# Performance work log

Hardware: AMD Instinct MI355X
Metric: run time of the kernel (lower is better)

## Reference

```python
import jax, jax.numpy as jnp
import numpy as np

B, T, N, H, F, E = 8, 64, 2048, 64, 64, 32768
G = 3 * H  # GRU gate dim


def setup_inputs() -> dict:
    key = jax.random.key(0)
    ks = jax.random.split(key, 12)
    s = 0.05
    return {
        "x": jax.random.normal(ks[0], (B, T, N, F), jnp.float32),
        "targets": jax.random.normal(ks[1], (B, T, N, 1), jnp.float32),
        "targets_mask": jax.random.uniform(ks[2], (B, T, N, 1)) > 0.2,
        "edge_index": jax.random.randint(ks[3], (2, E), 0, N),
        "W_msg": jax.random.normal(ks[4], (H, H), jnp.float32) * s,
        "b_msg": jnp.zeros((H,), jnp.float32),
        "W_mix": jax.random.normal(ks[5], (H, H + F), jnp.float32) * s,
        "b_mix": jnp.zeros((H,), jnp.float32),
        "W_ih": jax.random.normal(ks[6], (N, G, H), jnp.float32) * s,
        "W_hh": jax.random.normal(ks[7], (N, G, H), jnp.float32) * s,
        "b_ih": jnp.zeros((N, G), jnp.float32),
        "b_hh": jnp.zeros((N, G), jnp.float32),
        "W_read": jax.random.normal(ks[8], (1, H), jnp.float32) * s,
        "b_read": jnp.zeros((1,), jnp.float32),
    }


def reference(x, targets, targets_mask, edge_index,
              W_msg, b_msg, W_mix, b_mix,
              W_ih, W_hh, b_ih, b_hh, W_read, b_read):
    src, dst = edge_index[0], edge_index[1]

    def step(state, x_t):
        # state: [B,N,H], x_t: [B,N,F]
        m = jnp.einsum('bnh,gh->bng', state, W_msg) + b_msg           # state_to_message
        agg = jnp.zeros_like(m).at[:, dst, :].add(m[:, src, :])       # add-aggregate over directed edges
        mi = jnp.concatenate([agg, x_t], axis=-1)                     # [B,N,H+F]
        m2 = jnp.einsum('bnf,hf->bnh', mi, W_mix) + b_mix             # mix_input
        # per-node independent GRU cells (batched weights [N,3H,*])
        gi = jnp.einsum('bnh,ngh->bng', m2, W_ih) + b_ih
        gh = jnp.einsum('bnh,ngh->bng', state, W_hh) + b_hh
        i_r, i_z, i_n = jnp.split(gi, 3, axis=-1)
        h_r, h_z, h_n = jnp.split(gh, 3, axis=-1)
        r = jax.nn.sigmoid(i_r + h_r)
        z = jax.nn.sigmoid(i_z + h_z)
        n_cand = jnp.tanh(i_n + r * h_n)
        new_state = (1.0 - z) * n_cand + z * state
        out = jnp.einsum('bnh,oh->bno', new_state, W_read) + b_read   # readout -> [B,N,1]
        return new_state, out

    state0 = jnp.zeros((B, N, H), x.dtype)
    _, outs = jax.lax.scan(step, state0, jnp.swapaxes(x, 0, 1))       # outs: [T,B,N,1]
    outputs = jnp.swapaxes(outs, 0, 1)                                # [B,T,N,1]
    loss = 0.5 * (outputs - targets) ** 2
    mask = targets_mask.astype(loss.dtype)
    return jnp.sum(loss * mask) / jnp.sum(mask)                       # masked mean
```

## Files before the change

kernel.cpp:

```cpp
#include <hip/hip_runtime.h>
#include <math.h>

namespace {
constexpr int B = 8, T = 64, N = 2048, H = 64, F = 64, E = 32768, G = 192;
constexpr int BNH = B * N * H;
constexpr int NWELEM = N * G * H;
constexpr int NBLK = 1024;
}

typedef __attribute__((ext_vector_type(8))) short bfrag;
typedef __attribute__((ext_vector_type(4))) float ffrag;
typedef long f8frag;

#define MFMA(a, b, c)  __builtin_amdgcn_mfma_f32_16x16x32_bf16(a, b, c, 0, 0, 0)
#define MFMA8(a, b, c) __builtin_amdgcn_mfma_f32_16x16x32_fp8_fp8(a, b, c, 0, 0, 0)

#define DS (1.f / 512.f)

__device__ __forceinline__ unsigned short f2bf(float f) {
  unsigned u = __float_as_uint(f);
  u += 0x7fffu + ((u >> 16) & 1u);
  return (unsigned short)(u >> 16);
}
__device__ __forceinline__ float bf2f(unsigned short u) {
  return __uint_as_float(((unsigned)u) << 16);
}
template<bool HI>
__device__ __forceinline__ unsigned cvtpk8(float a, float b, unsigned old) {
  return __builtin_amdgcn_cvt_pk_fp8_f32(a, b, old, HI);
}

__device__ __forceinline__ void grid_bar(int* bar, int t) {
  __syncthreads();
  if (threadIdx.x == 0) {
    __hip_atomic_fetch_add(&bar[(blockIdx.x & 63) * 16], 1,
                           __ATOMIC_RELAXED, __HIP_MEMORY_SCOPE_AGENT);
  }
  if (blockIdx.x == 0) {
    if (threadIdx.x < 64) {
      while (__hip_atomic_load(&bar[threadIdx.x * 16],
                               __ATOMIC_RELAXED, __HIP_MEMORY_SCOPE_AGENT) < 16 * (t + 1))
        __builtin_amdgcn_s_sleep(1);
      if (threadIdx.x == 0)
        __hip_atomic_store(&bar[4096], t + 1, __ATOMIC_RELAXED, __HIP_MEMORY_SCOPE_AGENT);
    }
  } else if (threadIdx.x == 0) {
    while (__hip_atomic_load(&bar[4096], __ATOMIC_RELAXED, __HIP_MEMORY_SCOPE_AGENT) < t + 1)
      __builtin_amdgcn_s_sleep(2);
  }
  asm volatile("" ::: "memory");
  __syncthreads();
}


__global__ __launch_bounds__(256) void init_kernel(
    unsigned short* __restrict__ buf0, const float* __restrict__ b_msg,
    float* __restrict__ loss_acc, float* __restrict__ scal,
    int* __restrict__ deg, int* __restrict__ bar)
{
  int stride = gridDim.x * blockDim.x;
  for (int i = blockIdx.x * blockDim.x + threadIdx.x; i < BNH; i += stride) {
    buf0[i] = f2bf(b_msg[i & (H - 1)]);
    if (i < 8192) bar[i] = 0;
    if (i < N) { loss_acc[i] = 0.f; deg[i] = 0; }
    if (i < 16) scal[i] = 0.f;
  }
}

__global__ __launch_bounds__(256) void conv_kernel(
    const float* __restrict__ Wi, const float* __restrict__ Wh,
    const float* __restrict__ Wm, const float* __restrict__ Wg,
    unsigned char* __restrict__ Wib, unsigned char* __restrict__ Whb,
    unsigned short* __restrict__ Wmb, unsigned short* __restrict__ Wgb)
{
  int stride = gridDim.x * blockDim.x * 2;
  for (int i = (blockIdx.x * blockDim.x + threadIdx.x) * 2; i < NWELEM; i += stride) {
    unsigned p = cvtpk8<false>(Wi[i] * 32.f, Wi[i + 1] * 32.f, 0u);
    *(unsigned short*)(Wib + i) = (unsigned short)p;
    p = cvtpk8<false>(Wh[i] * 32.f, Wh[i + 1] * 32.f, 0u);
    *(unsigned short*)(Whb + i) = (unsigned short)p;
    if (i < 64 * 128) { Wmb[i] = f2bf(Wm[i]); Wmb[i + 1] = f2bf(Wm[i + 1]); }
    if (i < 64 * 64)  { Wgb[i] = f2bf(Wg[i]); Wgb[i + 1] = f2bf(Wg[i + 1]); }
  }
}

__global__ __launch_bounds__(256) void hist_kernel(const int* __restrict__ ei, int* __restrict__ deg) {
  int e = blockIdx.x * 256 + threadIdx.x;
  if (e < E) atomicAdd(&deg[ei[E + e]], 1);
}

__global__ __launch_bounds__(1024) void scan_kernel(const int* __restrict__ deg,
    int* __restrict__ row_ptr, int* __restrict__ cursor)
{
  __shared__ int s[N];
  int tid = threadIdx.x;
  s[tid] = deg[tid];
  s[tid + 1024] = deg[tid + 1024];
  __syncthreads();
  for (int off = 1; off < N; off <<= 1) {
    int v0 = (tid >= off) ? s[tid - off] : 0;
    int v1 = s[tid + 1024 - off];
    __syncthreads();
    s[tid] += v0;
    s[tid + 1024] += v1;
    __syncthreads();
  }
  row_ptr[tid + 1] = s[tid];
  row_ptr[tid + 1025] = s[tid + 1024];
  cursor[tid] = (tid == 0) ? 0 : s[tid - 1];
  cursor[tid + 1024] = s[tid + 1023];
  if (tid == 0) row_ptr[0] = 0;
}

__global__ __launch_bounds__(256) void fill_kernel(const int* __restrict__ ei,
    int* __restrict__ cursor, int* __restrict__ col_src)
{
  int e = blockIdx.x * 256 + threadIdx.x;
  if (e < E) {
    int d = ei[E + e];
    int slot = atomicAdd(&cursor[d], 1);
    col_src[slot] = ei[e];
  }
}

__global__ __launch_bounds__(256) void mask_kernel(const int* __restrict__ mask, float* __restrict__ scal) {
  int stride = gridDim.x * blockDim.x;
  int v = 0;
  for (int i = blockIdx.x * blockDim.x + threadIdx.x; i < B * T * N; i += stride)
    v += (mask[i] != 0);
  for (int o = 1; o < 64; o <<= 1) v += __shfl_xor(v, o, 64);
  if ((threadIdx.x & 63) == 0) atomicAdd(&scal[0], (float)v);
}


__global__ __attribute__((amdgpu_flat_work_group_size(256, 256), amdgpu_waves_per_eu(4, 4)))
void persist_kernel(
    const float* __restrict__ x, const float* __restrict__ targets,
    const int* __restrict__ mask,
    const unsigned char* __restrict__ W_ihb, const unsigned char* __restrict__ W_hhb,
    const unsigned short* __restrict__ W_mixb, const unsigned short* __restrict__ W_msgb,
    const float* __restrict__ b_ih, const float* __restrict__ b_hh,
    const float* __restrict__ b_mix, const float* __restrict__ b_msg,
    const float* __restrict__ W_read, const float* __restrict__ b_read,
    const int* __restrict__ row_ptr, const int* __restrict__ col_src,
    unsigned short* bufs,
    float* __restrict__ loss_acc, int* __restrict__ bar)
{
  __shared__ float sts[2][8][64];
  __shared__ float partial[4][8][72];
  __shared__ unsigned char m2F8[8 * 80];
  __shared__ unsigned short nsA[8 * 72];
  __shared__ float redS[4][8];

  const int tid = threadIdx.x;
  const int w = tid >> 6, lane = tid & 63;
  const int mrow = lane & 15, quad = lane >> 4;
  const int n0 = blockIdx.x * 2;
  const bfrag za = (bfrag)0;
  const int hcol = w * 16 + mrow;

  f8frag whf[2][6], wif[2][6];
#pragma unroll
  for (int k = 0; k < 2; ++k) {
    const unsigned char* Wh = W_hhb + (size_t)(n0 + k) * (G * H);
    const unsigned char* Wi = W_ihb + (size_t)(n0 + k) * (G * H);
#pragma unroll
    for (int tt = 0; tt < 3; ++tt) {
      const int off = ((w + tt * 4) * 16 + mrow) * H + quad * 8;
      whf[k][2 * tt]     = *(const f8frag*)(Wh + off);
      whf[k][2 * tt + 1] = *(const f8frag*)(Wh + off + 32);
      wif[k][2 * tt]     = *(const f8frag*)(Wi + off);
      wif[k][2 * tt + 1] = *(const f8frag*)(Wi + off + 32);
    }
  }
  const unsigned short* wmp = W_mixb + hcol * 128 + quad * 8;
  const unsigned short* wgp = W_msgb + hcol * H + quad * 8;

  float bir[2], biz[2], bin_[2], bhr[2], bhz[2], bhn[2];
#pragma unroll
  for (int k = 0; k < 2; ++k) {
    const int bg = (n0 + k) * G + hcol;
    bir[k] = b_ih[bg]; biz[k] = b_ih[bg + 64]; bin_[k] = b_ih[bg + 128];
    bhr[k] = b_hh[bg]; bhz[k] = b_hh[bg + 64]; bhn[k] = b_hh[bg + 128];
  }
  float wrd = W_read[hcol];
  float bmix = b_mix[hcol];
  float bmsg = b_msg[hcol];
  const float brd = b_read[0];
  const int e0a = row_ptr[n0], e0b = row_ptr[n0 + 1], e0c = row_ptr[n0 + 2];

#pragma unroll
  for (int k = 0; k < 2; ++k) {
#pragma unroll
    for (int j = 0; j < 6; ++j) {
      asm volatile("" : "+v"(whf[k][j]));
      asm volatile("" : "+v"(wif[k][j]));
    }
    asm volatile("" : "+v"(bir[k]), "+v"(biz[k]), "+v"(bin_[k]),
                      "+v"(bhr[k]), "+v"(bhz[k]), "+v"(bhn[k]));
  }
  asm volatile("" : "+v"(wrd), "+v"(bmix), "+v"(bmsg));

  for (int i = tid; i < 2 * 8 * 64; i += 256) ((float*)sts)[i] = 0.f;
  __syncthreads();

  float lsum[2] = {0.f, 0.f};
  const unsigned short* mcur = bufs;
  unsigned short* mnxt = bufs + BNH;

#pragma unroll 1
  for (int t = 0; t < T; ++t) {
#pragma unroll
    for (int k = 0; k < 2; ++k) {
      const int nn = n0 + k;
      const int ee0 = k ? e0b : e0a;
      const int ee1 = k ? e0c : e0b;

      bfrag wm0 = *(const bfrag*)(wmp);
      bfrag wm1 = *(const bfrag*)(wmp + 32);
      bfrag wm2 = *(const bfrag*)(wmp + 64);
      bfrag wm3 = *(const bfrag*)(wmp + 96);
      f8frag asF0 = 0, asF1 = 0;
      bfrag a2 = za, a3 = za;
      if (mrow < 8) {
        const float* sp = &sts[k][mrow][0];
        {
          float4 s0 = *(const float4*)(sp + quad * 8);
          float4 s1 = *(const float4*)(sp + quad * 8 + 4);
          unsigned u0 = 0, u1 = 0;
          u0 = cvtpk8<false>(s0.x * 16.f, s0.y * 16.f, u0);
          u0 = cvtpk8<true >(s0.z * 16.f, s0.w * 16.f, u0);
          u1 = cvtpk8<false>(s1.x * 16.f, s1.y * 16.f, u1);
          u1 = cvtpk8<true >(s1.z * 16.f, s1.w * 16.f, u1);
          asF0 = (f8frag)(((unsigned long long)u1 << 32) | u0);
          s0 = *(const float4*)(sp + 32 + quad * 8);
          s1 = *(const float4*)(sp + 32 + quad * 8 + 4);
          u0 = 0; u1 = 0;
          u0 = cvtpk8<false>(s0.x * 16.f, s0.y * 16.f, u0);
          u0 = cvtpk8<true >(s0.z * 16.f, s0.w * 16.f, u0);
          u1 = cvtpk8<false>(s1.x * 16.f, s1.y * 16.f, u1);
          u1 = cvtpk8<true >(s1.z * 16.f, s1.w * 16.f, u1);
          asF1 = (f8frag)(((unsigned long long)u1 << 32) | u0);
        }
        const float* xp = x + (((size_t)mrow * T + t) * N + nn) * F;
        {
          float4 t0 = *(const float4*)(xp + quad * 8);
          float4 t1 = *(const float4*)(xp + quad * 8 + 4);
          a2[0]=(short)f2bf(t0.x); a2[1]=(short)f2bf(t0.y); a2[2]=(short)f2bf(t0.z); a2[3]=(short)f2bf(t0.w);
          a2[4]=(short)f2bf(t1.x); a2[5]=(short)f2bf(t1.y); a2[6]=(short)f2bf(t1.z); a2[7]=(short)f2bf(t1.w);
          t0 = *(const float4*)(xp + 32 + quad * 8);
          t1 = *(const float4*)(xp + 32 + quad * 8 + 4);
          a3[0]=(short)f2bf(t0.x); a3[1]=(short)f2bf(t0.y); a3[2]=(short)f2bf(t0.z); a3[3]=(short)f2bf(t0.w);
          a3[4]=(short)f2bf(t1.x); a3[5]=(short)f2bf(t1.y); a3[6]=(short)f2bf(t1.z); a3[7]=(short)f2bf(t1.w);
        }
      }
      {
        float accL[4] = {0.f,0.f,0.f,0.f}, accH[4] = {0.f,0.f,0.f,0.f};
        const int j = lane & 31, bh = lane >> 5;
        const unsigned* mcU = (const unsigned*)mcur;
        for (int e = ee0 + w; e < ee1; e += 4) {
          const unsigned* mp = mcU + (size_t)col_src[e] * 256 + bh * 32 + j;
#pragma unroll
          for (int bb = 0; bb < 4; ++bb) {
            unsigned v = mp[bb * 64];
            accL[bb] += bf2f((unsigned short)(v & 0xffffu));
            accH[bb] += bf2f((unsigned short)(v >> 16));
          }
        }
#pragma unroll
        for (int bb = 0; bb < 4; ++bb) {
          partial[w][bb * 2 + bh][2 * j]     = accL[bb];
          partial[w][bb * 2 + bh][2 * j + 1] = accH[bb];
        }
      }
      ffrag ah0 = {0.f,0.f,0.f,0.f}, ah1 = {0.f,0.f,0.f,0.f}, ah2 = {0.f,0.f,0.f,0.f};
      ah0 = MFMA8(asF0, whf[k][0], ah0); ah0 = MFMA8(asF1, whf[k][1], ah0);
      ah1 = MFMA8(asF0, whf[k][2], ah1); ah1 = MFMA8(asF1, whf[k][3], ah1);
      ah2 = MFMA8(asF0, whf[k][4], ah2); ah2 = MFMA8(asF1, whf[k][5], ah2);
      __syncthreads();

      {
        bfrag a0 = za, a1 = za;
        if (mrow < 8) {
          const float* p = &partial[0][mrow][quad * 8];
#pragma unroll
          for (int j = 0; j < 8; ++j) {
            float s = p[j] + p[j + 576] + p[j + 1152] + p[j + 1728];
            a0[j] = (short)f2bf(s);
          }
          const float* p2 = &partial[0][mrow][32 + quad * 8];
#pragma unroll
          for (int j = 0; j < 8; ++j) {
            float s = p2[j] + p2[j + 576] + p2[j + 1152] + p2[j + 1728];
            a1[j] = (short)f2bf(s);
          }
        }
        ffrag accm = {0.f, 0.f, 0.f, 0.f};
        accm = MFMA(a0, wm0, accm);
        accm = MFMA(a1, wm1, accm);
        accm = MFMA(a2, wm2, accm);
        accm = MFMA(a3, wm3, accm);
        if (quad < 2) {
#pragma unroll
          for (int r = 0; r < 4; ++r) {
            unsigned p = cvtpk8<false>((accm[r] + bmix) * 16.f, 0.f, 0u);
            m2F8[(quad * 4 + r) * 80 + hcol] = (unsigned char)(p & 0xffu);
          }
        }
      }
      __syncthreads();

      bfrag wg0 = *(const bfrag*)(wgp);
      bfrag wg1 = *(const bfrag*)(wgp + 32);
      {
        f8frag amF0 = 0, amF1 = 0;
        if (mrow < 8) {
          amF0 = *(const f8frag*)&m2F8[mrow * 80 + quad * 8];
          amF1 = *(const f8frag*)&m2F8[mrow * 80 + 32 + quad * 8];
        }
        ffrag ai0 = {0.f,0.f,0.f,0.f}, ai1 = {0.f,0.f,0.f,0.f}, ai2 = {0.f,0.f,0.f,0.f};
        ai0 = MFMA8(amF0, wif[k][0], ai0); ai0 = MFMA8(amF1, wif[k][1], ai0);
        ai1 = MFMA8(amF0, wif[k][2], ai1); ai1 = MFMA8(amF1, wif[k][3], ai1);
        ai2 = MFMA8(amF0, wif[k][4], ai2); ai2 = MFMA8(amF1, wif[k][5], ai2);
        if (quad < 2) {
          float v[4];
#pragma unroll
          for (int r = 0; r < 4; ++r) {
            const int b = quad * 4 + r;
            float rs  = (ai0[r] + ah0[r]) * DS + bir[k] + bhr[k];
            float zs  = (ai1[r] + ah1[r]) * DS + biz[k] + bhz[k];
            float in_ = ai2[r] * DS + bin_[k];
            float hn  = ah2[r] * DS + bhn[k];
            float rg = 1.f / (1.f + __expf(-rs));
            float z  = 1.f / (1.f + __expf(-zs));
            float pre = in_ + rg * hn;
            float a = __expf(-2.f * fabsf(pre));
            float nc = copysignf((1.f - a) / (1.f + a), pre);
            float sold = sts[k][b][hcol];
            float ns = (1.f - z) * nc + z * sold;
            sts[k][b][hcol] = ns;
            nsA[b * 72 + hcol] = f2bf(ns);
            v[r] = ns * wrd;
          }
#pragma unroll
          for (int o = 1; o < 16; o <<= 1) {
#pragma unroll
            for (int r = 0; r < 4; ++r) v[r] += __shfl_xor(v[r], o, 64);
          }
          if (mrow == 0) {
#pragma unroll
            for (int r = 0; r < 4; ++r) redS[w][quad * 4 + r] = v[r];
          }
        }
      }
      __syncthreads();

      {
        bfrag an0 = za, an1 = za;
        if (mrow < 8) {
          an0 = *(const bfrag*)&nsA[mrow * 72 + quad * 8];
          an1 = *(const bfrag*)&nsA[mrow * 72 + 32 + quad * 8];
        }
        ffrag accg = {0.f, 0.f, 0.f, 0.f};
        accg = MFMA(an0, wg0, accg);
        accg = MFMA(an1, wg1, accg);
        if (quad < 2) {
          unsigned* mnU = (unsigned*)mnxt;
          const int jcol = hcol >> 1;
#pragma unroll
          for (int r = 0; r < 4; ++r) {
            float v0 = accg[r] + bmsg;
            float v1 = __shfl_xor(v0, 1, 64);
            if (!(mrow & 1)) {
              unsigned pk = (unsigned)f2bf(v0) | ((unsigned)f2bf(v1) << 16);
              __hip_atomic_store(&mnU[(size_t)nn * 256 + (quad * 4 + r) * 32 + jcol],
                                 pk, __ATOMIC_RELAXED, __HIP_MEMORY_SCOPE_AGENT);
            }
          }
        }
      }
      if (tid < 8) {
        float vv = redS[0][tid] + redS[1][tid] + redS[2][tid] + redS[3][tid] + brd;
        size_t idx = ((size_t)tid * T + t) * N + nn;
        float d = vv - targets[idx];
        float l = (mask[idx] != 0) ? 0.5f * d * d : 0.f;
        l += __shfl_xor(l, 1, 64);
        l += __shfl_xor(l, 2, 64);
        l += __shfl_xor(l, 4, 64);
        if (tid == 0) lsum[k] += l;
      }
    }
    grid_bar(bar, t);
    mcur = mnxt;
    mnxt += BNH;
  }
  if (tid == 0) { loss_acc[n0] = lsum[0]; loss_acc[n0 + 1] = lsum[1]; }
}

__global__ __launch_bounds__(256) void final_kernel(const float* __restrict__ loss_acc,
    const float* __restrict__ scal, float* __restrict__ out)
{
  __shared__ float sred[4];
  float v = 0.f;
  for (int i = threadIdx.x; i < N; i += 256) v += loss_acc[i];
  for (int o = 1; o < 64; o <<= 1) v += __shfl_xor(v, o, 64);
  if ((threadIdx.x & 63) == 0) sred[threadIdx.x >> 6] = v;
  __syncthreads();
  if (threadIdx.x == 0) out[0] = (sred[0] + sred[1] + sred[2] + sred[3]) / scal[0];
}

extern "C" void kernel_launch(void* const* d_in, const int* in_sizes, int n_in,
                              void* d_out, int out_size, void* d_ws, size_t ws_size,
                              hipStream_t stream)
{
  const float* x       = (const float*)d_in[0];
  const float* targets = (const float*)d_in[1];
  const int*   mask    = (const int*)d_in[2];
  const int*   ei      = (const int*)d_in[3];
  const float* W_msg   = (const float*)d_in[4];
  const float* b_msg   = (const float*)d_in[5];
  const float* W_mix   = (const float*)d_in[6];
  const float* b_mix   = (const float*)d_in[7];
  const float* W_ih    = (const float*)d_in[8];
  const float* W_hh    = (const float*)d_in[9];
  const float* b_ih    = (const float*)d_in[10];
  const float* b_hh    = (const float*)d_in[11];
  const float* W_read  = (const float*)d_in[12];
  const float* b_read  = (const float*)d_in[13];
  float* out = (float*)d_out;

  unsigned short* bufs  = (unsigned short*)d_ws;
  float* loss_acc       = (float*)(bufs + (size_t)(T + 1) * BNH);
  float* scal           = loss_acc + N;
  int* deg              = (int*)(scal + 16);
  int* row_ptr          = deg + N;
  int* cursor           = row_ptr + (N + 16);
  int* col_src          = cursor + N;
  int* bar              = col_src + E;
  unsigned char* W_ihb  = (unsigned char*)(bar + 8192);
  unsigned char* W_hhb  = W_ihb + NWELEM;
  unsigned short* W_mixb = (unsigned short*)(W_hhb + NWELEM);
  unsigned short* W_msgb = W_mixb + 64 * 128;

  init_kernel<<<1024, 256, 0, stream>>>(bufs, b_msg, loss_acc, scal, deg, bar);
  conv_kernel<<<8192, 256, 0, stream>>>(W_ih, W_hh, W_mix, W_msg, W_ihb, W_hhb, W_mixb, W_msgb);
  hist_kernel<<<E / 256, 256, 0, stream>>>(ei, deg);
  scan_kernel<<<1, 1024, 0, stream>>>(deg, row_ptr, cursor);
  fill_kernel<<<E / 256, 256, 0, stream>>>(ei, cursor, col_src);
  mask_kernel<<<512, 256, 0, stream>>>(mask, scal);

  persist_kernel<<<NBLK, 256, 0, stream>>>(x, targets, mask,
                                           W_ihb, W_hhb, W_mixb, W_msgb,
                                           b_ih, b_hh, b_mix, b_msg, W_read, b_read,
                                           row_ptr, col_src, bufs, loss_acc, bar);

  final_kernel<<<1, 256, 0, stream>>>(loss_acc, scal, out);
}
```

Before: 2.180 ms.

## Process both nodes per block together to halve block barriers per step

Restructures each time step so the two nodes a block owns are processed in lockstep, with double-buffered shared staging (m2F8, nsA, redS). Each phase now covers both nodes, cutting the __syncthreads count per step from six to three. Edge gathering is split so two waves serve each node, and the x loads for both nodes are issued at the start of the step. The cost is higher register pressure from holding both nodes' fragments and accumulators, at a fixed 4-waves-per-EU occupancy.

```diff
diff --git a/kernel.cpp b/kernel.cpp
--- a/kernel.cpp
+++ b/kernel.cpp
@@ -148,9 +148,9 @@
 {
   __shared__ float sts[2][8][64];
   __shared__ float partial[4][8][72];
-  __shared__ unsigned char m2F8[8 * 80];
-  __shared__ unsigned short nsA[8 * 72];
-  __shared__ float redS[4][8];
+  __shared__ unsigned char m2F8[2][8 * 80];
+  __shared__ unsigned short nsA[2][8 * 72];
+  __shared__ float redS[2][4][8];
 
   const int tid = threadIdx.x;
   const int w = tid >> 6, lane = tid & 63;
@@ -204,162 +204,179 @@
   for (int i = tid; i < 2 * 8 * 64; i += 256) ((float*)sts)[i] = 0.f;
   __syncthreads();
 
-  float lsum[2] = {0.f, 0.f};
+  float lsum0 = 0.f, lsum1 = 0.f;
   const unsigned short* mcur = bufs;
   unsigned short* mnxt = bufs + BNH;
 
 #pragma unroll 1
   for (int t = 0; t < T; ++t) {
+    float4 xt[2][4];
+    if (mrow < 8) {
+#pragma unroll
+      for (int k = 0; k < 2; ++k) {
+        const float* xp = x + (((size_t)mrow * T + t) * N + (n0 + k)) * F;
+        xt[k][0] = *(const float4*)(xp + quad * 8);
+        xt[k][1] = *(const float4*)(xp + quad * 8 + 4);
+        xt[k][2] = *(const float4*)(xp + 32 + quad * 8);
+        xt[k][3] = *(const float4*)(xp + 32 + quad * 8 + 4);
+      }
+    }
+    {
+      const int kk = w >> 1, ws = w & 1;
+      const int ge0 = (kk ? e0b : e0a) + ws;
+      const int ge1 = kk ? e0c : e0b;
+      float accL[4] = {0.f,0.f,0.f,0.f}, accH[4] = {0.f,0.f,0.f,0.f};
+      const int j = lane & 31, bh = lane >> 5;
+      const unsigned* mcU = (const unsigned*)mcur;
+      for (int e = ge0; e < ge1; e += 2) {
+        const unsigned* mp = mcU + (size_t)col_src[e] * 256 + bh * 32 + j;
+#pragma unroll
+        for (int bb = 0; bb < 4; ++bb) {
+          unsigned v = mp[bb * 64];
+          accL[bb] += bf2f((unsigned short)(v & 0xffffu));
+          accH[bb] += bf2f((unsigned short)(v >> 16));
+        }
+      }
+#pragma unroll
+      for (int bb = 0; bb < 4; ++bb) {
+        partial[w][bb * 2 + bh][2 * j]     = accL[bb];
+        partial[w][bb * 2 + bh][2 * j + 1] = accH[bb];
+      }
+    }
+    f8frag asF[2][2];
+    bfrag a2[2], a3[2];
+#pragma unroll
+    for (int k = 0; k < 2; ++k) { asF[k][0] = 0; asF[k][1] = 0; a2[k] = za; a3[k] = za; }
+    if (mrow < 8) {
+#pragma unroll
+      for (int k = 0; k < 2; ++k) {
+        const float* sp = &sts[k][mrow][0];
+        float4 s0 = *(const float4*)(sp + quad * 8);
+        float4 s1 = *(const float4*)(sp + quad * 8 + 4);
+        unsigned u0 = 0, u1 = 0;
+        u0 = cvtpk8<false>(s0.x * 16.f, s0.y * 16.f, u0);
+        u0 = cvtpk8<true >(s0.z * 16.f, s0.w * 16.f, u0);
+        u1 = cvtpk8<false>(s1.x * 16.f, s1.y * 16.f, u1);
+        u1 = cvtpk8<true >(s1.z * 16.f, s1.w * 16.f, u1);
+        asF[k][0] = (f8frag)(((unsigned long long)u1 << 32) | u0);
+        s0 = *(const float4*)(sp + 32 + quad * 8);
+        s1 = *(const float4*)(sp + 32 + quad * 8 + 4);
+        u0 = 0; u1 = 0;
+        u0 = cvtpk8<false>(s0.x * 16.f, s0.y * 16.f, u0);
+        u0 = cvtpk8<true >(s0.z * 16.f, s0.w * 16.f, u0);
+        u1 = cvtpk8<false>(s1.x * 16.f, s1.y * 16.f, u1);
+        u1 = cvtpk8<true >(s1.z * 16.f, s1.w * 16.f, u1);
+        asF[k][1] = (f8frag)(((unsigned long long)u1 << 32) | u0);
+        a2[k][0]=(short)f2bf(xt[k][0].x); a2[k][1]=(short)f2bf(xt[k][0].y);
+        a2[k][2]=(short)f2bf(xt[k][0].z); a2[k][3]=(short)f2bf(xt[k][0].w);
+        a2[k][4]=(short)f2bf(xt[k][1].x); a2[k][5]=(short)f2bf(xt[k][1].y);
+        a2[k][6]=(short)f2bf(xt[k][1].z); a2[k][7]=(short)f2bf(xt[k][1].w);
+        a3[k][0]=(short)f2bf(xt[k][2].x); a3[k][1]=(short)f2bf(xt[k][2].y);
+        a3[k][2]=(short)f2bf(xt[k][2].z); a3[k][3]=(short)f2bf(xt[k][2].w);
+        a3[k][4]=(short)f2bf(xt[k][3].x); a3[k][5]=(short)f2bf(xt[k][3].y);
+        a3[k][6]=(short)f2bf(xt[k][3].z); a3[k][7]=(short)f2bf(xt[k][3].w);
+      }
+    }
+    ffrag ah[2][3];
 #pragma unroll
     for (int k = 0; k < 2; ++k) {
-      const int nn = n0 + k;
-      const int ee0 = k ? e0b : e0a;
-      const int ee1 = k ? e0c : e0b;
-
+      ah[k][0] = (ffrag){0.f,0.f,0.f,0.f};
+      ah[k][1] = (ffrag){0.f,0.f,0.f,0.f};
+      ah[k][2] = (ffrag){0.f,0.f,0.f,0.f};
+      ah[k][0] = MFMA8(asF[k][0], whf[k][0], ah[k][0]);
+      ah[k][0] = MFMA8(asF[k][1], whf[k][1], ah[k][0]);
+      ah[k][1] = MFMA8(asF[k][0], whf[k][2], ah[k][1]);
+      ah[k][1] = MFMA8(asF[k][1], whf[k][3], ah[k][1]);
+      ah[k][2] = MFMA8(asF[k][0], whf[k][4], ah[k][2]);
+      ah[k][2] = MFMA8(asF[k][1], whf[k][5], ah[k][2]);
+    }
+    __syncthreads();
+
+    {
       bfrag wm0 = *(const bfrag*)(wmp);
       bfrag wm1 = *(const bfrag*)(wmp + 32);
       bfrag wm2 = *(const bfrag*)(wmp + 64);
       bfrag wm3 = *(const bfrag*)(wmp + 96);
-      f8frag asF0 = 0, asF1 = 0;
-      bfrag a2 = za, a3 = za;
-      if (mrow < 8) {
-        const float* sp = &sts[k][mrow][0];
-        {
-          float4 s0 = *(const float4*)(sp + quad * 8);
-          float4 s1 = *(const float4*)(sp + quad * 8 + 4);
-          unsigned u0 = 0, u1 = 0;
-          u0 = cvtpk8<false>(s0.x * 16.f, s0.y * 16.f, u0);
-          u0 = cvtpk8<true >(s0.z * 16.f, s0.w * 16.f, u0);
-          u1 = cvtpk8<false>(s1.x * 16.f, s1.y * 16.f, u1);
-          u1 = cvtpk8<true >(s1.z * 16.f, s1.w * 16.f, u1);
-          asF0 = (f8frag)(((unsigned long long)u1 << 32) | u0);
-          s0 = *(const float4*)(sp + 32 + quad * 8);
-          s1 = *(const float4*)(sp + 32 + quad * 8 + 4);
-          u0 = 0; u1 = 0;
-          u0 = cvtpk8<false>(s0.x * 16.f, s0.y * 16.f, u0);
-          u0 = cvtpk8<true >(s0.z * 16.f, s0.w * 16.f, u0);
-          u1 = cvtpk8<false>(s1.x * 16.f, s1.y * 16.f, u1);
-          u1 = cvtpk8<true >(s1.z * 16.f, s1.w * 16.f, u1);
-          asF1 = (f8frag)(((unsigned long long)u1 << 32) | u0);
-        }
-        const float* xp = x + (((size_t)mrow * T + t) * N + nn) * F;
-        {
-          float4 t0 = *(const float4*)(xp + quad * 8);
-          float4 t1 = *(const float4*)(xp + quad * 8 + 4);
-          a2[0]=(short)f2bf(t0.x); a2[1]=(short)f2bf(t0.y); a2[2]=(short)f2bf(t0.z); a2[3]=(short)f2bf(t0.w);
-          a2[4]=(short)f2bf(t1.x); a2[5]=(short)f2bf(t1.y); a2[6]=(short)f2bf(t1.z); a2[7]=(short)f2bf(t1.w);
-          t0 = *(const float4*)(xp + 32 + quad * 8);
-          t1 = *(const float4*)(xp + 32 + quad * 8 + 4);
-          a3[0]=(short)f2bf(t0.x); a3[1]=(short)f2bf(t0.y); a3[2]=(short)f2bf(t0.z); a3[3]=(short)f2bf(t0.w);
-          a3[4]=(short)f2bf(t1.x); a3[5]=(short)f2bf(t1.y); a3[6]=(short)f2bf(t1.z); a3[7]=(short)f2bf(t1.w);
-        }
-      }
-      {
-        float accL[4] = {0.f,0.f,0.f,0.f}, accH[4] = {0.f,0.f,0.f,0.f};
-        const int j = lane & 31, bh = lane >> 5;
-        const unsigned* mcU = (const unsigned*)mcur;
-        for (int e = ee0 + w; e < ee1; e += 4) {
-          const unsigned* mp = mcU + (size_t)col_src[e] * 256 + bh * 32 + j;
-#pragma unroll
-          for (int bb = 0; bb < 4; ++bb) {
-            unsigned v = mp[bb * 64];
-            accL[bb] += bf2f((unsigned short)(v & 0xffffu));
-            accH[bb] += bf2f((unsigned short)(v >> 16));
-          }
-        }
-#pragma unroll
-        for (int bb = 0; bb < 4; ++bb) {
-          partial[w][bb * 2 + bh][2 * j]     = accL[bb];
-          partial[w][bb * 2 + bh][2 * j + 1] = accH[bb];
-        }
-      }
-      ffrag ah0 = {0.f,0.f,0.f,0.f}, ah1 = {0.f,0.f,0.f,0.f}, ah2 = {0.f,0.f,0.f,0.f};
-      ah0 = MFMA8(asF0, whf[k][0], ah0); ah0 = MFMA8(asF1, whf[k][1], ah0);
-      ah1 = MFMA8(asF0, whf[k][2], ah1); ah1 = MFMA8(asF1, whf[k][3], ah1);
-      ah2 = MFMA8(asF0, whf[k][4], ah2); ah2 = MFMA8(asF1, whf[k][5], ah2);
-      __syncthreads();
-
-      {
+#pragma unroll
+      for (int k = 0; k < 2; ++k) {
         bfrag a0 = za, a1 = za;
         if (mrow < 8) {
-          const float* p = &partial[0][mrow][quad * 8];
-#pragma unroll
-          for (int j = 0; j < 8; ++j) {
-            float s = p[j] + p[j + 576] + p[j + 1152] + p[j + 1728];
-            a0[j] = (short)f2bf(s);
-          }
-          const float* p2 = &partial[0][mrow][32 + quad * 8];
-#pragma unroll
-          for (int j = 0; j < 8; ++j) {
-            float s = p2[j] + p2[j + 576] + p2[j + 1152] + p2[j + 1728];
-            a1[j] = (short)f2bf(s);
-          }
+          const float* p = &partial[2 * k][mrow][quad * 8];
+#pragma unroll
+          for (int j = 0; j < 8; ++j) a0[j] = (short)f2bf(p[j] + p[j + 576]);
+          const float* p2 = &partial[2 * k][mrow][32 + quad * 8];
+#pragma unroll
+          for (int j = 0; j < 8; ++j) a1[j] = (short)f2bf(p2[j] + p2[j + 576]);
         }
         ffrag accm = {0.f, 0.f, 0.f, 0.f};
         accm = MFMA(a0, wm0, accm);
         accm = MFMA(a1, wm1, accm);
-        accm = MFMA(a2, wm2, accm);
-        accm = MFMA(a3, wm3, accm);
+        accm = MFMA(a2[k], wm2, accm);
+        accm = MFMA(a3[k], wm3, accm);
         if (quad < 2) {
 #pragma unroll
           for (int r = 0; r < 4; ++r) {
             unsigned p = cvtpk8<false>((accm[r] + bmix) * 16.f, 0.f, 0u);
-            m2F8[(quad * 4 + r) * 80 + hcol] = (unsigned char)(p & 0xffu);
+            m2F8[k][(quad * 4 + r) * 80 + hcol] = (unsigned char)(p & 0xffu);
           }
         }
       }
-      __syncthreads();
-
+    }
+    __syncthreads();
+
+#pragma unroll
+    for (int k = 0; k < 2; ++k) {
+      f8frag amF0 = 0, amF1 = 0;
+      if (mrow < 8) {
+        amF0 = *(const f8frag*)&m2F8[k][mrow * 80 + quad * 8];
+        amF1 = *(const f8frag*)&m2F8[k][mrow * 80 + 32 + quad * 8];
+      }
+      ffrag ai0 = {0.f,0.f,0.f,0.f}, ai1 = {0.f,0.f,0.f,0.f}, ai2 = {0.f,0.f,0.f,0.f};
+      ai0 = MFMA8(amF0, wif[k][0], ai0); ai0 = MFMA8(amF1, wif[k][1], ai0);
+      ai1 = MFMA8(amF0, wif[k][2], ai1); ai1 = MFMA8(amF1, wif[k][3], ai1);
+      ai2 = MFMA8(amF0, wif[k][4], ai2); ai2 = MFMA8(amF1, wif[k][5], ai2);
+      if (quad < 2) {
+        float v[4];
+#pragma unroll
+        for (int r = 0; r < 4; ++r) {
+          const int b = quad * 4 + r;
+          float rs  = (ai0[r] + ah[k][0][r]) * DS + bir[k] + bhr[k];
+          float zs  = (ai1[r] + ah[k][1][r]) * DS + biz[k] + bhz[k];
+          float in_ = ai2[r] * DS + bin_[k];
+          float hn  = ah[k][2][r] * DS + bhn[k];
+          float rg = 1.f / (1.f + __expf(-rs));
+          float z  = 1.f / (1.f + __expf(-zs));
+          float pre = in_ + rg * hn;
+          float a = __expf(-2.f * fabsf(pre));
+          float nc = copysignf((1.f - a) / (1.f + a), pre);
+          float sold = sts[k][b][hcol];
+          float ns = (1.f - z) * nc + z * sold;
+          sts[k][b][hcol] = ns;
+          nsA[k][b * 72 + hcol] = f2bf(ns);
+          v[r] = ns * wrd;
+        }
+#pragma unroll
+        for (int o = 1; o < 16; o <<= 1) {
+#pragma unroll
+          for (int r = 0; r < 4; ++r) v[r] += __shfl_xor(v[r], o, 64);
+        }
+        if (mrow == 0) {
+#pragma unroll
+          for (int r = 0; r < 4; ++r) redS[k][w][quad * 4 + r] = v[r];
+        }
+      }
+    }
+    __syncthreads();
+
+    {
       bfrag wg0 = *(const bfrag*)(wgp);
       bfrag wg1 = *(const bfrag*)(wgp + 32);
-      {
-        f8frag amF0 = 0, amF1 = 0;
-        if (mrow < 8) {
-          amF0 = *(const f8frag*)&m2F8[mrow * 80 + quad * 8];
-          amF1 = *(const f8frag*)&m2F8[mrow * 80 + 32 + quad * 8];
-        }
-        ffrag ai0 = {0.f,0.f,0.f,0.f}, ai1 = {0.f,0.f,0.f,0.f}, ai2 = {0.f,0.f,0.f,0.f};
-        ai0 = MFMA8(amF0, wif[k][0], ai0); ai0 = MFMA8(amF1, wif[k][1], ai0);
-        ai1 = MFMA8(amF0, wif[k][2], ai1); ai1 = MFMA8(amF1, wif[k][3], ai1);
-        ai2 = MFMA8(amF0, wif[k][4], ai2); ai2 = MFMA8(amF1, wif[k][5], ai2);
-        if (quad < 2) {
-          float v[4];
-#pragma unroll
-          for (int r = 0; r < 4; ++r) {
-            const int b = quad * 4 + r;
-            float rs  = (ai0[r] + ah0[r]) * DS + bir[k] + bhr[k];
-            float zs  = (ai1[r] + ah1[r]) * DS + biz[k] + bhz[k];
-            float in_ = ai2[r] * DS + bin_[k];
-            float hn  = ah2[r] * DS + bhn[k];
-            float rg = 1.f / (1.f + __expf(-rs));
-            float z  = 1.f / (1.f + __expf(-zs));
-            float pre = in_ + rg * hn;
-            float a = __expf(-2.f * fabsf(pre));
-            float nc = copysignf((1.f - a) / (1.f + a), pre);
-            float sold = sts[k][b][hcol];
-            float ns = (1.f - z) * nc + z * sold;
-            sts[k][b][hcol] = ns;
-            nsA[b * 72 + hcol] = f2bf(ns);
-            v[r] = ns * wrd;
-          }
-#pragma unroll
-          for (int o = 1; o < 16; o <<= 1) {
-#pragma unroll
-            for (int r = 0; r < 4; ++r) v[r] += __shfl_xor(v[r], o, 64);
-          }
-          if (mrow == 0) {
-#pragma unroll
-            for (int r = 0; r < 4; ++r) redS[w][quad * 4 + r] = v[r];
-          }
-        }
-      }
-      __syncthreads();
-
-      {
+#pragma unroll
+      for (int k = 0; k < 2; ++k) {
         bfrag an0 = za, an1 = za;
         if (mrow < 8) {
-          an0 = *(const bfrag*)&nsA[mrow * 72 + quad * 8];
-          an1 = *(const bfrag*)&nsA[mrow * 72 + 32 + quad * 8];
+          an0 = *(const bfrag*)&nsA[k][mrow * 72 + quad * 8];
+          an1 = *(const bfrag*)&nsA[k][mrow * 72 + 32 + quad * 8];
         }
         ffrag accg = {0.f, 0.f, 0.f, 0.f};
         accg = MFMA(an0, wg0, accg);
@@ -373,28 +390,31 @@
             float v1 = __shfl_xor(v0, 1, 64);
             if (!(mrow & 1)) {
               unsigned pk = (unsigned)f2bf(v0) | ((unsigned)f2bf(v1) << 16);
-              __hip_atomic_store(&mnU[(size_t)nn * 256 + (quad * 4 + r) * 32 + jcol],
+              __hip_atomic_store(&mnU[(size_t)(n0 + k) * 256 + (quad * 4 + r) * 32 + jcol],
                                  pk, __ATOMIC_RELAXED, __HIP_MEMORY_SCOPE_AGENT);
             }
           }
         }
       }
-      if (tid < 8) {
-        float vv = redS[0][tid] + redS[1][tid] + redS[2][tid] + redS[3][tid] + brd;
-        size_t idx = ((size_t)tid * T + t) * N + nn;
-        float d = vv - targets[idx];
-        float l = (mask[idx] != 0) ? 0.5f * d * d : 0.f;
-        l += __shfl_xor(l, 1, 64);
-        l += __shfl_xor(l, 2, 64);
-        l += __shfl_xor(l, 4, 64);
-        if (tid == 0) lsum[k] += l;
-      }
+    }
+    if (tid < 16) {
+      const int k = tid >> 3, b = tid & 7;
+      float vv = redS[k][0][b] + redS[k][1][b] + redS[k][2][b] + redS[k][3][b] + brd;
+      size_t idx = ((size_t)b * T + t) * N + (n0 + k);
+      float d = vv - targets[idx];
+      float l = (mask[idx] != 0) ? 0.5f * d * d : 0.f;
+      l += __shfl_xor(l, 1, 64);
+      l += __shfl_xor(l, 2, 64);
+      l += __shfl_xor(l, 4, 64);
+      if (tid == 0) lsum0 += l;
+      if (tid == 8) lsum1 += l;
     }
     grid_bar(bar, t);
     mcur = mnxt;
     mnxt += BNH;
   }
-  if (tid == 0) { loss_acc[n0] = lsum[0]; loss_acc[n0 + 1] = lsum[1]; }
+  if (tid == 0) loss_acc[n0] = lsum0;
+  if (tid == 8) loss_acc[n0 + 1] = lsum1;
 }
 
 __global__ __launch_bounds__(256) void final_kernel(const float* __restrict__ loss_acc,
```

New measurement: 3.328 ms. 1.53x slower.
